# Kernel optimization log

Hardware: AMD Instinct MI355X
Metric: run time of the kernel (lower is better)

Reference implementation:

```python
import jax, jax.numpy as jnp
import numpy as np
from jax.scipy.special import erf

B, S, D = 8, 512, 512
H = 8            # num_heads per half
DH = D // 2      # 256, per-branch model dim
DFF = 2048
HOUT = 2


def _layernorm(x, g, b, eps=1e-6):
    mu = jnp.mean(x, axis=-1, keepdims=True)
    var = jnp.mean(jnp.square(x - mu), axis=-1, keepdims=True)
    return (x - mu) / jnp.sqrt(var + eps) * g + b


def _rescale_dist(w):
    one = jnp.float32(1.0)
    return (one + jnp.exp(one)) / (one + jnp.exp(one - w))


def _mha(xin, wq, bq, wk, bk, wv, bv, wo, bo, maskf, adjoin, dist):
    b, s, dm = xin.shape
    dep = dm // H
    def heads(t):
        return t.reshape(b, s, H, dep).transpose(0, 2, 1, 3)  # (b,h,s,dep)
    q = heads(xin @ wq + bq)
    k = heads(xin @ wk + bk)
    v = heads(xin @ wv + bv)
    scores = jnp.einsum('bhqd,bhkd->bhqk', q, k)
    scale = jnp.sqrt(jnp.float32(dep))
    if dist is not None:
        scores = jax.nn.relu(scores) * _rescale_dist(dist) / scale
    else:
        scores = scores / scale
    scores = scores + maskf * jnp.float32(-1e9)
    if adjoin is not None:
        scores = scores + adjoin
    attn = jax.nn.softmax(scores, axis=-1)
    out = jnp.einsum('bhqk,bhkd->bhqd', attn, v).transpose(0, 2, 1, 3).reshape(b, s, dm)
    return out @ wo + bo, attn


def setup_inputs() -> dict:
    key = jax.random.key(0)
    ks = jax.random.split(key, 32)
    init = lambda k, shp: (jax.random.normal(k, shp, dtype=jnp.float32) * 0.02)
    inp = {
        'x': jax.random.normal(ks[0], (B, S, D), dtype=jnp.float32),
        'adjoin_matrix': jax.random.normal(ks[1], (B, 1, S, S), dtype=jnp.float32),
        'dist_matrix': jax.random.uniform(ks[2], (B, 1, S, S), dtype=jnp.float32),
        # mha1 (adjoin branch)
        'wq1': init(ks[3], (DH, DH)), 'bq1': jnp.zeros((DH,), jnp.float32),
        'wk1': init(ks[4], (DH, DH)), 'bk1': jnp.zeros((DH,), jnp.float32),
        'wv1': init(ks[5], (DH, DH)), 'bv1': jnp.zeros((DH,), jnp.float32),
        'wo1': init(ks[6], (DH, DH)), 'bo1': jnp.zeros((DH,), jnp.float32),
        # mha2 (distance branch)
        'wq2': init(ks[7], (DH, DH)), 'bq2': jnp.zeros((DH,), jnp.float32),
        'wk2': init(ks[8], (DH, DH)), 'bk2': jnp.zeros((DH,), jnp.float32),
        'wv2': init(ks[9], (DH, DH)), 'bv2': jnp.zeros((DH,), jnp.float32),
        'wo2': init(ks[10], (DH, DH)), 'bo2': jnp.zeros((DH,), jnp.float32),
        # BANLayer
        'vnet_w': init(ks[11], (DH, 2 * DH)), 'vnet_b': jnp.zeros((2 * DH,), jnp.float32),
        'qnet_w': init(ks[12], (DH, 2 * DH)), 'qnet_b': jnp.zeros((2 * DH,), jnp.float32),
        'h_mat': init(ks[13], (1, HOUT, 1, 2 * DH)),
        'h_bias': init(ks[14], (1, HOUT, 1, 1)),
        'bn_gamma': jnp.ones((D,), jnp.float32), 'bn_beta': jnp.zeros((D,), jnp.float32),
        'bn_mean': jnp.zeros((D,), jnp.float32), 'bn_var': jnp.ones((D,), jnp.float32),
        # LayerNorms
        'ln1_g': jnp.ones((D,), jnp.float32), 'ln1_b': jnp.zeros((D,), jnp.float32),
        'ln2_g': jnp.ones((D,), jnp.float32), 'ln2_b': jnp.zeros((D,), jnp.float32),
        # FFN
        'ffn_w1': init(ks[15], (D, DFF)), 'ffn_b1': jnp.zeros((DFF,), jnp.float32),
        'ffn_w2': init(ks[16], (DFF, D)), 'ffn_b2': jnp.zeros((D,), jnp.float32),
        # padding mask (int -> cast), 1 = masked
        'encoder_padding_mask': jax.random.randint(ks[17], (B, 1, 1, S), 0, 2, dtype=jnp.int32),
    }
    return inp


def reference(x, adjoin_matrix, dist_matrix,
              wq1, bq1, wk1, bk1, wv1, bv1, wo1, bo1,
              wq2, bq2, wk2, bk2, wv2, bv2, wo2, bo2,
              vnet_w, vnet_b, qnet_w, qnet_b, h_mat, h_bias,
              bn_gamma, bn_beta, bn_mean, bn_var,
              ln1_g, ln1_b, ln2_g, ln2_b,
              ffn_w1, ffn_b1, ffn_w2, ffn_b2,
              encoder_padding_mask):
    maskf = encoder_padding_mask.astype(jnp.float32)
    x1, x2 = jnp.split(x, 2, axis=-1)
    # local branch: adjoin bias, no distance
    x_l, aw_local = _mha(x1, wq1, bq1, wk1, bk1, wv1, bv1, wo1, bo1, maskf, adjoin_matrix, None)
    # global branch: relu + distance rescale, no adjoin
    x_g, aw_global = _mha(x2, wq2, bq2, wk2, bk2, wv2, bv2, wo2, bo2, maskf, None, dist_matrix)
    # BANLayer (h_out=2 <= c, eval mode; p_net is identity for rows=1)
    v_ = jax.nn.relu(x_l @ vnet_w + vnet_b)   # (B,S,2*DH)
    q_ = jax.nn.relu(x_g @ qnet_w + qnet_b)
    att_maps = jnp.einsum('xhyk,bvk,bqk->bhvq', h_mat, v_, q_) + h_bias  # (B,HOUT,S,S)
    logits = jnp.einsum('bvk,bhvq,bqk->bvk', v_, att_maps, q_)           # sum over h
    logits = (logits - bn_mean) / jnp.sqrt(bn_var + 1e-3) * bn_gamma + bn_beta
    attn_output = logits * jnp.concatenate([x_l, x_g], axis=-1)
    out1 = _layernorm(x + attn_output, ln1_g, ln1_b)
    h = out1 @ ffn_w1 + ffn_b1
    h = 0.5 * h * (1.0 + erf(h / jnp.sqrt(jnp.float32(2.0))))  # exact gelu
    ffn_out = h @ ffn_w2 + ffn_b2
    out2 = _layernorm(out1 + ffn_out, ln2_g, ln2_b)
    return (out2, aw_local, aw_global)
```

## Files before the change

### kernel.cpp

```cpp
#include <hip/hip_runtime.h>
#include <hip/hip_bf16.h>

typedef __hip_bfloat16 bf16;
typedef __attribute__((ext_vector_type(8))) short bf16x8;
typedef __attribute__((ext_vector_type(4))) float f32x4;

#define BB 8
#define SS 512
#define DD 512
#define NH 8
#define DHm 256
#define DEP 32
#define DFF 2048

__device__ __forceinline__ bf16x8 cvt8(const float* p) {
  union { bf16x8 v; bf16 h[8]; } u;
  float4 f0 = *(const float4*)p, f1 = *(const float4*)(p + 4);
  u.h[0]=__float2bfloat16(f0.x); u.h[1]=__float2bfloat16(f0.y);
  u.h[2]=__float2bfloat16(f0.z); u.h[3]=__float2bfloat16(f0.w);
  u.h[4]=__float2bfloat16(f1.x); u.h[5]=__float2bfloat16(f1.y);
  u.h[6]=__float2bfloat16(f1.z); u.h[7]=__float2bfloat16(f1.w);
  return u.v;
}

template<typename TA, bool TRANSB, int ACT, typename TC>
__global__ __launch_bounds__(256)
void mfma_gemm(const TA* __restrict__ A, const float* __restrict__ B,
               const float* __restrict__ bias, TC* __restrict__ C,
               int M, int N, int K, int lda, int ldb, int ldc,
               long long sA, long long sB, long long sC)
{
  __shared__ bf16 As[64][32];
  __shared__ bf16 Bs[64][32];
  const int t = threadIdx.x;
  const int lane = t & 63, wave = t >> 6;
  const int wm = (wave & 1) << 5, wn = (wave >> 1) << 5;
  const int l15 = lane & 15, quad = lane >> 4;
  const int row0 = blockIdx.y << 6, col0 = blockIdx.x << 6;
  const TA* Ab = A + (long long)blockIdx.z * sA;
  const float* Bb = B + (long long)blockIdx.z * sB;
  TC* Cb = C + (long long)blockIdx.z * sC;

  const int ar  = t >> 2, acb = t & 3;
  const int aswz = ((acb ^ ((ar >> 1) & 3)) << 3);
  const int bn  = t & 63, bkb = t >> 6;
  const int bswz = ((bkb ^ ((bn >> 1) & 3)) << 3);

  f32x4 acc[2][2] = {};

  for (int k0 = 0; k0 < K; k0 += 32) {
    {
      union { bf16x8 v; bf16 h[8]; } u;
      if constexpr (sizeof(TA) == 2) {
        u.v = *(const bf16x8*)&Ab[(long long)(row0 + ar) * lda + k0 + (acb << 3)];
      } else {
        u.v = cvt8((const float*)&Ab[(long long)(row0 + ar) * lda + k0 + (acb << 3)]);
      }
      *(bf16x8*)&As[ar][aswz] = u.v;
    }
    if (TRANSB) {
      *(bf16x8*)&Bs[ar][aswz] = cvt8(&Bb[(long long)(col0 + ar) * ldb + k0 + (acb << 3)]);
    } else {
      union { bf16x8 v; bf16 h[8]; } u;
#pragma unroll
      for (int j = 0; j < 8; j++)
        u.h[j] = __float2bfloat16(Bb[(long long)(k0 + (bkb << 3) + j) * ldb + col0 + bn]);
      *(bf16x8*)&Bs[bn][bswz] = u.v;
    }
    __syncthreads();
    bf16x8 afr[2], bfr[2];
#pragma unroll
    for (int i = 0; i < 2; i++) {
      int m = wm + (i << 4) + l15;
      afr[i] = *(bf16x8*)&As[m][((quad ^ ((m >> 1) & 3)) << 3)];
      int n = wn + (i << 4) + l15;
      bfr[i] = *(bf16x8*)&Bs[n][((quad ^ ((n >> 1) & 3)) << 3)];
    }
#pragma unroll
    for (int i = 0; i < 2; i++)
#pragma unroll
      for (int j = 0; j < 2; j++)
        acc[i][j] = __builtin_amdgcn_mfma_f32_16x16x32_bf16(afr[i], bfr[j], acc[i][j], 0, 0, 0);
    __syncthreads();
  }

#pragma unroll
  for (int i = 0; i < 2; i++) {
#pragma unroll
    for (int j = 0; j < 2; j++) {
      int col = col0 + wn + (j << 4) + l15;
      float bv = bias ? bias[col] : 0.f;
#pragma unroll
      for (int r = 0; r < 4; r++) {
        int row = row0 + wm + (i << 4) + (quad << 2) + r;
        float v = acc[i][j][r] + bv;
        if (ACT == 1) v = fmaxf(v, 0.f);
        if (ACT == 2) v = 0.5f * v * (1.f + erff(v * 0.70710678118654752f));
        if constexpr (sizeof(TC) == 2) Cb[(long long)row * ldc + col] = __float2bfloat16(v);
        else                           Cb[(long long)row * ldc + col] = v;
      }
    }
  }
}

template<int BRANCH>
__global__ __launch_bounds__(256, 2)
void attn_mfma(const float* __restrict__ QKV, const int* __restrict__ mask,
               const float* __restrict__ extra, float* __restrict__ aw,
               float* __restrict__ ctx)
{
  const int qt = blockIdx.x, h = blockIdx.y, b = blockIdx.z;
  const int t = threadIdx.x, lane = t & 63, wave = t >> 6;
  const int l15 = lane & 15, quad = lane >> 4;
  __shared__ bf16x8 Vt[64][32];

  {
    const float* Vb = QKV + (long long)b * SS * 768 + 512 + h * 32;
    int dep = t & 31;
#pragma unroll
    for (int j8 = 0; j8 < 8; j8++) {
      int blk = (t >> 5) + (j8 << 3);
      union { bf16x8 v; bf16 hh[8]; } u;
#pragma unroll
      for (int i = 0; i < 8; i++)
        u.hh[i] = __float2bfloat16(Vb[(long long)(blk * 8 + i) * 768 + dep]);
      Vt[blk][dep] = u.v;
    }
  }

  const int q0 = qt * 64 + wave * 16;
  const float* Qb = QKV + ((long long)(b * SS + q0)) * 768 + h * 32;
  bf16x8 qfrag = cvt8(Qb + (long long)l15 * 768 + quad * 8);
  __syncthreads();

  const float scale_inv = 0.17677669529663688f;
  const float* Kb = QKV + (long long)b * SS * 768 + 256 + h * 32;
  const float* Eb = extra + ((long long)b * SS + q0) * SS;
  float sreg[32][4];
  float rmax[4] = {-1e30f, -1e30f, -1e30f, -1e30f};
#pragma unroll
  for (int kc = 0; kc < 32; kc++) {
    int kpos = kc * 16 + l15;
    bf16x8 kfrag = cvt8(Kb + (long long)kpos * 768 + quad * 8);
    f32x4 a = __builtin_amdgcn_mfma_f32_16x16x32_bf16(qfrag, kfrag, f32x4{0.f,0.f,0.f,0.f}, 0, 0, 0);
    float mval = (float)mask[b * SS + kpos] * -1e9f;
#pragma unroll
    for (int r = 0; r < 4; r++) {
      float s = a[r];
      float ev = Eb[(long long)(quad * 4 + r) * SS + kpos];
      if (BRANCH == 1) {
        s = s * scale_inv + mval + ev;
      } else {
        float resc = 3.7182818284590452f / (1.f + __expf(1.f - ev));
        s = fmaxf(s, 0.f) * resc * scale_inv + mval;
      }
      sreg[kc][r] = s;
      rmax[r] = fmaxf(rmax[r], s);
    }
  }
#pragma unroll
  for (int r = 0; r < 4; r++) {
    float v = rmax[r];
    v = fmaxf(v, __shfl_xor(v, 1, 16));
    v = fmaxf(v, __shfl_xor(v, 2, 16));
    v = fmaxf(v, __shfl_xor(v, 4, 16));
    v = fmaxf(v, __shfl_xor(v, 8, 16));
    rmax[r] = v;
  }
  float rsum[4] = {0.f, 0.f, 0.f, 0.f};
#pragma unroll
  for (int kc = 0; kc < 32; kc++)
#pragma unroll
    for (int r = 0; r < 4; r++) {
      float e = __expf(sreg[kc][r] - rmax[r]);
      sreg[kc][r] = e;
      rsum[r] += e;
    }
#pragma unroll
  for (int r = 0; r < 4; r++) {
    float v = rsum[r];
    v += __shfl_xor(v, 1, 16);
    v += __shfl_xor(v, 2, 16);
    v += __shfl_xor(v, 4, 16);
    v += __shfl_xor(v, 8, 16);
    rsum[r] = 1.f / v;
  }
  float* awp = aw + (((long long)(b * NH + h) * SS + q0)) * SS;
#pragma unroll
  for (int kc = 0; kc < 32; kc++)
#pragma unroll
    for (int r = 0; r < 4; r++)
      awp[(long long)(quad * 4 + r) * SS + kc * 16 + l15] = sreg[kc][r] * rsum[r];

  asm volatile("s_waitcnt vmcnt(0)" ::: "memory");

  f32x4 oacc[2] = {};
#pragma unroll
  for (int kc2 = 0; kc2 < 16; kc2++) {
    bf16x8 afr = cvt8(awp + (long long)l15 * SS + kc2 * 32 + quad * 8);
#pragma unroll
    for (int n = 0; n < 2; n++) {
      bf16x8 bfr = Vt[kc2 * 4 + quad][n * 16 + l15];
      oacc[n] = __builtin_amdgcn_mfma_f32_16x16x32_bf16(afr, bfr, oacc[n], 0, 0, 0);
    }
  }
#pragma unroll
  for (int n = 0; n < 2; n++)
#pragma unroll
    for (int r = 0; r < 4; r++) {
      int q = q0 + quad * 4 + r;
      ctx[(long long)(b * SS + q) * DHm + h * 32 + n * 16 + l15] = oacc[n][r];
    }
}

__global__ __launch_bounds__(256)
void pack_qkv(const float* __restrict__ wq, const float* __restrict__ wk,
              const float* __restrict__ wv, const float* __restrict__ bq,
              const float* __restrict__ bk, const float* __restrict__ bv,
              float* __restrict__ WB, float* __restrict__ BBo)
{
  int idx = blockIdx.x * 256 + threadIdx.x;
  if (idx < 768 * 256) {
    int k = idx / 768, c = idx % 768;
    int part = c >> 8, n = c & 255;
    const float* w = part == 0 ? wq : (part == 1 ? wk : wv);
    WB[idx] = w[k * 256 + n];
  } else if (idx < 768 * 256 + 768) {
    int c = idx - 768 * 256;
    int part = c >> 8, n = c & 255;
    const float* bs = part == 0 ? bq : (part == 1 ? bk : bv);
    BBo[c] = bs[n];
  }
}

__global__ __launch_bounds__(256)
void vh_kernel(const float* __restrict__ v_, const float* __restrict__ hmat,
               float* __restrict__ vh, int n)
{
  int i = blockIdx.x * 256 + threadIdx.x;
  if (i < n) {
    int c = i & (DD - 1);
    vh[i] = v_[i] * (hmat[c] + hmat[DD + c]);
  }
}

__global__ __launch_bounds__(256)
void addhb_kernel(float* __restrict__ G, const float* __restrict__ hb, int n)
{
  int i = blockIdx.x * 256 + threadIdx.x;
  if (i < n) G[i] += hb[0] + hb[1];
}

__global__ __launch_bounds__(256)
void bn_gate_ln1_kernel(const float* __restrict__ x, const float* __restrict__ vbuf,
                        const float* __restrict__ T, const float* __restrict__ xl,
                        const float* __restrict__ xg,
                        const float* __restrict__ bng, const float* __restrict__ bnb,
                        const float* __restrict__ bnm, const float* __restrict__ bnv,
                        const float* __restrict__ lng, const float* __restrict__ lnb,
                        float* __restrict__ out1)
{
  const int row = blockIdx.x;
  const int t = threadIdx.x;
  __shared__ float red[256];
  float val[2];
#pragma unroll
  for (int i = 0; i < 2; i++) {
    int c = t + i * 256;
    long long idx = (long long)row * DD + c;
    float lg = vbuf[idx] * T[idx];
    float bn = (lg - bnm[c]) / sqrtf(bnv[c] + 1e-3f) * bng[c] + bnb[c];
    float gate = (c < DHm) ? xl[(long long)row * DHm + c] : xg[(long long)row * DHm + (c - DHm)];
    val[i] = x[idx] + bn * gate;
  }
  red[t] = val[0] + val[1];
  __syncthreads();
  for (int o = 128; o > 0; o >>= 1) { if (t < o) red[t] += red[t + o]; __syncthreads(); }
  float mu = red[0] * (1.f / 512.f);
  __syncthreads();
  float d0 = val[0] - mu, d1 = val[1] - mu;
  red[t] = d0 * d0 + d1 * d1;
  __syncthreads();
  for (int o = 128; o > 0; o >>= 1) { if (t < o) red[t] += red[t + o]; __syncthreads(); }
  float inv = 1.f / sqrtf(red[0] * (1.f / 512.f) + 1e-6f);
  out1[(long long)row * DD + t]       = d0 * inv * lng[t]       + lnb[t];
  out1[(long long)row * DD + t + 256] = d1 * inv * lng[t + 256] + lnb[t + 256];
}

__global__ __launch_bounds__(256)
void ln2_kernel(const float* __restrict__ a, const float* __restrict__ b2,
                const float* __restrict__ g, const float* __restrict__ bta,
                float* __restrict__ out)
{
  const int row = blockIdx.x;
  const int t = threadIdx.x;
  __shared__ float red[256];
  float v0 = a[(long long)row * DD + t]       + b2[(long long)row * DD + t];
  float v1 = a[(long long)row * DD + t + 256] + b2[(long long)row * DD + t + 256];
  red[t] = v0 + v1;
  __syncthreads();
  for (int o = 128; o > 0; o >>= 1) { if (t < o) red[t] += red[t + o]; __syncthreads(); }
  float mu = red[0] * (1.f / 512.f);
  __syncthreads();
  float d0 = v0 - mu, d1 = v1 - mu;
  red[t] = d0 * d0 + d1 * d1;
  __syncthreads();
  for (int o = 128; o > 0; o >>= 1) { if (t < o) red[t] += red[t + o]; __syncthreads(); }
  float inv = 1.f / sqrtf(red[0] * (1.f / 512.f) + 1e-6f);
  out[(long long)row * DD + t]       = d0 * inv * g[t]       + bta[t];
  out[(long long)row * DD + t + 256] = d1 * inv * g[t + 256] + bta[t + 256];
}

extern "C" void kernel_launch(void* const* d_in, const int* in_sizes, int n_in,
                              void* d_out, int out_size, void* d_ws, size_t ws_size,
                              hipStream_t stream) {
  const float* x      = (const float*)d_in[0];
  const float* adjoin = (const float*)d_in[1];
  const float* dist   = (const float*)d_in[2];
  const float* wq1=(const float*)d_in[3],  *bq1=(const float*)d_in[4];
  const float* wk1=(const float*)d_in[5],  *bk1=(const float*)d_in[6];
  const float* wv1=(const float*)d_in[7],  *bv1=(const float*)d_in[8];
  const float* wo1=(const float*)d_in[9],  *bo1=(const float*)d_in[10];
  const float* wq2=(const float*)d_in[11], *bq2=(const float*)d_in[12];
  const float* wk2=(const float*)d_in[13], *bk2=(const float*)d_in[14];
  const float* wv2=(const float*)d_in[15], *bv2=(const float*)d_in[16];
  const float* wo2=(const float*)d_in[17], *bo2=(const float*)d_in[18];
  const float* vnet_w=(const float*)d_in[19], *vnet_b=(const float*)d_in[20];
  const float* qnet_w=(const float*)d_in[21], *qnet_b=(const float*)d_in[22];
  const float* h_mat=(const float*)d_in[23], *h_bias=(const float*)d_in[24];
  const float* bn_g=(const float*)d_in[25], *bn_b=(const float*)d_in[26];
  const float* bn_m=(const float*)d_in[27], *bn_v=(const float*)d_in[28];
  const float* ln1_g=(const float*)d_in[29], *ln1_b=(const float*)d_in[30];
  const float* ln2_g=(const float*)d_in[31], *ln2_b=(const float*)d_in[32];
  const float* ffn_w1=(const float*)d_in[33], *ffn_b1=(const float*)d_in[34];
  const float* ffn_w2=(const float*)d_in[35], *ffn_b2=(const float*)d_in[36];
  const int* mask = (const int*)d_in[37];

  float* ws = (float*)d_ws;
  const long long M1 = 1048576LL;
  float* QKV1 = ws + 0 * M1;
  float* QKV2 = ws + 3 * M1;
  float* CTX  = ws + 6 * M1;
  float* XL   = ws + 7 * M1;
  float* XG   = ws + 8 * M1;
  float* Vn   = ws + 9 * M1;
  float* Qn   = ws + 11 * M1;
  float* WB1  = ws + 13 * M1;
  float* BB1v = WB1 + 196608;
  float* WB2  = BB1v + 768;
  float* BB2v = WB2 + 196608;
  float* VH   = ws + 0 * M1;
  float* G    = ws + 3 * M1;
  float* T    = ws + 13 * M1;
  float* OUT1 = ws + 0 * M1;
  bf16*  H    = (bf16*)(ws + 3 * M1);
  float* FFNO = ws + 7 * M1;

  float* out2 = (float*)d_out;
  float* awl  = out2 + 2097152LL;
  float* awg  = awl + 16777216LL;

  const int MROWS = BB * SS;
  const long long GST = (long long)SS * SS;

  pack_qkv<<<dim3(771), 256, 0, stream>>>(wq1, wk1, wv1, bq1, bk1, bv1, WB1, BB1v);
  pack_qkv<<<dim3(771), 256, 0, stream>>>(wq2, wk2, wv2, bq2, bk2, bv2, WB2, BB2v);

  mfma_gemm<float,false,0,float><<<dim3(768/64, MROWS/64, 1), 256, 0, stream>>>(
      x, WB1, BB1v, QKV1, MROWS, 768, DHm, DD, 768, 768, 0,0,0);
  attn_mfma<1><<<dim3(8, NH, BB), 256, 0, stream>>>(QKV1, mask, adjoin, awl, CTX);
  mfma_gemm<float,false,0,float><<<dim3(DHm/64, MROWS/64, 1), 256, 0, stream>>>(
      CTX, wo1, bo1, XL, MROWS, DHm, DHm, DHm, DHm, DHm, 0,0,0);

  mfma_gemm<float,false,0,float><<<dim3(768/64, MROWS/64, 1), 256, 0, stream>>>(
      x + DHm, WB2, BB2v, QKV2, MROWS, 768, DHm, DD, 768, 768, 0,0,0);
  attn_mfma<2><<<dim3(8, NH, BB), 256, 0, stream>>>(QKV2, mask, dist, awg, CTX);
  mfma_gemm<float,false,0,float><<<dim3(DHm/64, MROWS/64, 1), 256, 0, stream>>>(
      CTX, wo2, bo2, XG, MROWS, DHm, DHm, DHm, DHm, DHm, 0,0,0);

  mfma_gemm<float,false,1,float><<<dim3(DD/64, MROWS/64, 1), 256, 0, stream>>>(
      XL, vnet_w, vnet_b, Vn, MROWS, DD, DHm, DHm, DD, DD, 0,0,0);
  mfma_gemm<float,false,1,float><<<dim3(DD/64, MROWS/64, 1), 256, 0, stream>>>(
      XG, qnet_w, qnet_b, Qn, MROWS, DD, DHm, DHm, DD, DD, 0,0,0);
  vh_kernel<<<dim3((MROWS*DD)/256), 256, 0, stream>>>(Vn, h_mat, VH, MROWS*DD);
  mfma_gemm<float,true,0,float><<<dim3(SS/64, SS/64, BB), 256, 0, stream>>>(
      VH, Qn, (const float*)nullptr, G, SS, SS, DD, DD, DD, SS, GST, GST, GST);
  addhb_kernel<<<dim3((BB*SS*SS)/256), 256, 0, stream>>>(G, h_bias, BB*SS*SS);
  mfma_gemm<float,false,0,float><<<dim3(DD/64, SS/64, BB), 256, 0, stream>>>(
      G, Qn, (const float*)nullptr, T, SS, DD, SS, SS, DD, DD, GST, GST, GST);

  bn_gate_ln1_kernel<<<dim3(MROWS), 256, 0, stream>>>(
      x, Vn, T, XL, XG, bn_g, bn_b, bn_m, bn_v, ln1_g, ln1_b, OUT1);

  mfma_gemm<float,false,2,bf16><<<dim3(DFF/64, MROWS/64, 1), 256, 0, stream>>>(
      OUT1, ffn_w1, ffn_b1, H, MROWS, DFF, DD, DD, DFF, DFF, 0,0,0);
  mfma_gemm<bf16,false,0,float><<<dim3(DD/64, MROWS/64, 1), 256, 0, stream>>>(
      H, ffn_w2, ffn_b2, FFNO, MROWS, DD, DFF, DFF, DD, DD, 0,0,0);

  ln2_kernel<<<dim3(MROWS), 256, 0, stream>>>(OUT1, FFNO, ln2_g, ln2_b, out2);
}
```

Before: 528.7 us.

## Convert pipeline to bf16 intermediates with pre-transposed weights and direct-to-LDS GEMM loads

Replaces the fp32-input GEMM with a bf16 GEMM that loads A and B tiles straight into LDS using global_load_lds. All weights and x are converted and transposed to bf16 in one pack kernel. Intermediates (QKV, ctx, Vn, Qn, G, H) are now stored as bf16, which halves memory traffic and removes per-load conversions and strided B loads. The h_bias add is folded into a GEMM epilogue, and the large GEMMs get 128x128 tiles. The cost is an extra transpose kernel for Qn and more rounding error, notably with G held in bf16.

```diff
diff --git a/kernel.cpp b/kernel.cpp
--- a/kernel.cpp
+++ b/kernel.cpp
@@ -10,8 +10,12 @@
 #define DD 512
 #define NH 8
 #define DHm 256
-#define DEP 32
 #define DFF 2048
+
+__device__ __forceinline__ void gl_lds16(const void* g, void* l) {
+  __builtin_amdgcn_global_load_lds((const __attribute__((address_space(1))) void*)g,
+                                   (__attribute__((address_space(3))) void*)l, 16, 0, 0);
+}
 
 __device__ __forceinline__ bf16x8 cvt8(const float* p) {
   union { bf16x8 v; bf16 h[8]; } u;
@@ -23,91 +27,75 @@
   return u.v;
 }
 
-template<typename TA, bool TRANSB, int ACT, typename TC>
-__global__ __launch_bounds__(256)
-void mfma_gemm(const TA* __restrict__ A, const float* __restrict__ B,
-               const float* __restrict__ bias, TC* __restrict__ C,
-               int M, int N, int K, int lda, int ldb, int ldc,
-               long long sA, long long sB, long long sC)
-{
-  __shared__ bf16 As[64][32];
-  __shared__ bf16 Bs[64][32];
-  const int t = threadIdx.x;
-  const int lane = t & 63, wave = t >> 6;
-  const int wm = (wave & 1) << 5, wn = (wave >> 1) << 5;
+template<int BM, int BN, int SMODE, int BIASM, int ACT>
+__global__ __launch_bounds__(256)
+void gemm2(const bf16* __restrict__ A, const bf16* __restrict__ B,
+           const float* __restrict__ bias, float* __restrict__ Cf,
+           bf16* __restrict__ Cb, int K, int lda, int ldb, int ldc,
+           long long sA, long long sB, long long sC)
+{
+  __shared__ bf16 As[BM * 32];
+  __shared__ bf16 Bs[BN * 32];
+  const int t = threadIdx.x, lane = t & 63, wave = t >> 6;
   const int l15 = lane & 15, quad = lane >> 4;
-  const int row0 = blockIdx.y << 6, col0 = blockIdx.x << 6;
-  const TA* Ab = A + (long long)blockIdx.z * sA;
-  const float* Bb = B + (long long)blockIdx.z * sB;
-  TC* Cb = C + (long long)blockIdx.z * sC;
-
-  const int ar  = t >> 2, acb = t & 3;
-  const int aswz = ((acb ^ ((ar >> 1) & 3)) << 3);
-  const int bn  = t & 63, bkb = t >> 6;
-  const int bswz = ((bkb ^ ((bn >> 1) & 3)) << 3);
-
-  f32x4 acc[2][2] = {};
+  constexpr int WMT = BM / 32, WNT = BN / 32;
+  const int wm = (wave & 1) * (BM / 2), wn = (wave >> 1) * (BN / 2);
+  const int row0 = blockIdx.y * BM, col0 = blockIdx.x * BN;
+  const bf16* Ab = A + (long long)blockIdx.z * sA + (long long)row0 * lda;
+  const bf16* Bb = B + (long long)blockIdx.z * sB + (long long)col0 * ldb;
+  const int srow = wave * 16 + (lane >> 2), skc = (lane & 3) << 3;
+
+  f32x4 acc[WMT][WNT] = {};
 
   for (int k0 = 0; k0 < K; k0 += 32) {
-    {
-      union { bf16x8 v; bf16 h[8]; } u;
-      if constexpr (sizeof(TA) == 2) {
-        u.v = *(const bf16x8*)&Ab[(long long)(row0 + ar) * lda + k0 + (acb << 3)];
-      } else {
-        u.v = cvt8((const float*)&Ab[(long long)(row0 + ar) * lda + k0 + (acb << 3)]);
-      }
-      *(bf16x8*)&As[ar][aswz] = u.v;
-    }
-    if (TRANSB) {
-      *(bf16x8*)&Bs[ar][aswz] = cvt8(&Bb[(long long)(col0 + ar) * ldb + k0 + (acb << 3)]);
-    } else {
-      union { bf16x8 v; bf16 h[8]; } u;
-#pragma unroll
-      for (int j = 0; j < 8; j++)
-        u.h[j] = __float2bfloat16(Bb[(long long)(k0 + (bkb << 3) + j) * ldb + col0 + bn]);
-      *(bf16x8*)&Bs[bn][bswz] = u.v;
-    }
+#pragma unroll
+    for (int j = 0; j < BM / 64; j++)
+      gl_lds16(Ab + (long long)(srow + j * 64) * lda + k0 + skc,
+               (char*)As + wave * 1024 + j * 4096);
+#pragma unroll
+    for (int j = 0; j < BN / 64; j++)
+      gl_lds16(Bb + (long long)(srow + j * 64) * ldb + k0 + skc,
+               (char*)Bs + wave * 1024 + j * 4096);
     __syncthreads();
-    bf16x8 afr[2], bfr[2];
-#pragma unroll
-    for (int i = 0; i < 2; i++) {
-      int m = wm + (i << 4) + l15;
-      afr[i] = *(bf16x8*)&As[m][((quad ^ ((m >> 1) & 3)) << 3)];
-      int n = wn + (i << 4) + l15;
-      bfr[i] = *(bf16x8*)&Bs[n][((quad ^ ((n >> 1) & 3)) << 3)];
-    }
-#pragma unroll
-    for (int i = 0; i < 2; i++)
-#pragma unroll
-      for (int j = 0; j < 2; j++)
-        acc[i][j] = __builtin_amdgcn_mfma_f32_16x16x32_bf16(afr[i], bfr[j], acc[i][j], 0, 0, 0);
+    bf16x8 af[WMT], bfr[WNT];
+#pragma unroll
+    for (int i = 0; i < WMT; i++) af[i]  = *(const bf16x8*)&As[(wm + i * 16 + l15) * 32 + quad * 8];
+#pragma unroll
+    for (int j = 0; j < WNT; j++) bfr[j] = *(const bf16x8*)&Bs[(wn + j * 16 + l15) * 32 + quad * 8];
+#pragma unroll
+    for (int i = 0; i < WMT; i++)
+#pragma unroll
+      for (int j = 0; j < WNT; j++)
+        acc[i][j] = __builtin_amdgcn_mfma_f32_16x16x32_bf16(af[i], bfr[j], acc[i][j], 0, 0, 0);
     __syncthreads();
   }
 
-#pragma unroll
-  for (int i = 0; i < 2; i++) {
-#pragma unroll
-    for (int j = 0; j < 2; j++) {
-      int col = col0 + wn + (j << 4) + l15;
-      float bv = bias ? bias[col] : 0.f;
+  float sb = 0.f;
+  if (BIASM == 2) sb = bias[0] + bias[1];
+#pragma unroll
+  for (int i = 0; i < WMT; i++)
+#pragma unroll
+    for (int j = 0; j < WNT; j++) {
+      int col = col0 + wn + j * 16 + l15;
+      float bv = (BIASM == 1) ? bias[col] : sb;
 #pragma unroll
       for (int r = 0; r < 4; r++) {
-        int row = row0 + wm + (i << 4) + (quad << 2) + r;
+        int row = row0 + wm + i * 16 + (quad << 2) + r;
         float v = acc[i][j][r] + bv;
         if (ACT == 1) v = fmaxf(v, 0.f);
         if (ACT == 2) v = 0.5f * v * (1.f + erff(v * 0.70710678118654752f));
-        if constexpr (sizeof(TC) == 2) Cb[(long long)row * ldc + col] = __float2bfloat16(v);
-        else                           Cb[(long long)row * ldc + col] = v;
+        long long ci = (long long)blockIdx.z * sC + (long long)row * ldc + col;
+        if (SMODE & 1) Cf[ci] = v;
+        if (SMODE & 2) Cb[ci] = __float2bfloat16(v);
       }
     }
-  }
 }
 
 template<int BRANCH>
 __global__ __launch_bounds__(256, 2)
-void attn_mfma(const float* __restrict__ QKV, const int* __restrict__ mask,
+void attn_mfma(const bf16* __restrict__ QKV, const int* __restrict__ mask,
                const float* __restrict__ extra, float* __restrict__ aw,
-               float* __restrict__ ctx)
+               bf16* __restrict__ ctx)
 {
   const int qt = blockIdx.x, h = blockIdx.y, b = blockIdx.z;
   const int t = threadIdx.x, lane = t & 63, wave = t >> 6;
@@ -115,7 +103,7 @@
   __shared__ bf16x8 Vt[64][32];
 
   {
-    const float* Vb = QKV + (long long)b * SS * 768 + 512 + h * 32;
+    const bf16* Vb = QKV + (long long)b * SS * 768 + 512 + h * 32;
     int dep = t & 31;
 #pragma unroll
     for (int j8 = 0; j8 < 8; j8++) {
@@ -123,25 +111,25 @@
       union { bf16x8 v; bf16 hh[8]; } u;
 #pragma unroll
       for (int i = 0; i < 8; i++)
-        u.hh[i] = __float2bfloat16(Vb[(long long)(blk * 8 + i) * 768 + dep]);
+        u.hh[i] = Vb[(long long)(blk * 8 + i) * 768 + dep];
       Vt[blk][dep] = u.v;
     }
   }
 
   const int q0 = qt * 64 + wave * 16;
-  const float* Qb = QKV + ((long long)(b * SS + q0)) * 768 + h * 32;
-  bf16x8 qfrag = cvt8(Qb + (long long)l15 * 768 + quad * 8);
+  const bf16* Qb = QKV + ((long long)(b * SS + q0)) * 768 + h * 32;
+  bf16x8 qfrag = *(const bf16x8*)(Qb + (long long)l15 * 768 + quad * 8);
   __syncthreads();
 
   const float scale_inv = 0.17677669529663688f;
-  const float* Kb = QKV + (long long)b * SS * 768 + 256 + h * 32;
+  const bf16* Kb = QKV + (long long)b * SS * 768 + 256 + h * 32;
   const float* Eb = extra + ((long long)b * SS + q0) * SS;
   float sreg[32][4];
   float rmax[4] = {-1e30f, -1e30f, -1e30f, -1e30f};
 #pragma unroll
   for (int kc = 0; kc < 32; kc++) {
     int kpos = kc * 16 + l15;
-    bf16x8 kfrag = cvt8(Kb + (long long)kpos * 768 + quad * 8);
+    bf16x8 kfrag = *(const bf16x8*)(Kb + (long long)kpos * 768 + quad * 8);
     f32x4 a = __builtin_amdgcn_mfma_f32_16x16x32_bf16(qfrag, kfrag, f32x4{0.f,0.f,0.f,0.f}, 0, 0, 0);
     float mval = (float)mask[b * SS + kpos] * -1e9f;
 #pragma unroll
@@ -209,56 +197,102 @@
 #pragma unroll
     for (int r = 0; r < 4; r++) {
       int q = q0 + quad * 4 + r;
-      ctx[(long long)(b * SS + q) * DHm + h * 32 + n * 16 + l15] = oacc[n][r];
-    }
-}
-
-__global__ __launch_bounds__(256)
-void pack_qkv(const float* __restrict__ wq, const float* __restrict__ wk,
-              const float* __restrict__ wv, const float* __restrict__ bq,
-              const float* __restrict__ bk, const float* __restrict__ bv,
-              float* __restrict__ WB, float* __restrict__ BBo)
-{
-  int idx = blockIdx.x * 256 + threadIdx.x;
-  if (idx < 768 * 256) {
-    int k = idx / 768, c = idx % 768;
-    int part = c >> 8, n = c & 255;
-    const float* w = part == 0 ? wq : (part == 1 ? wk : wv);
-    WB[idx] = w[k * 256 + n];
-  } else if (idx < 768 * 256 + 768) {
-    int c = idx - 768 * 256;
-    int part = c >> 8, n = c & 255;
-    const float* bs = part == 0 ? bq : (part == 1 ? bk : bv);
-    BBo[c] = bs[n];
-  }
-}
-
-__global__ __launch_bounds__(256)
-void vh_kernel(const float* __restrict__ v_, const float* __restrict__ hmat,
-               float* __restrict__ vh, int n)
+      ctx[(long long)(b * SS + q) * DHm + h * 32 + n * 16 + l15] = __float2bfloat16(oacc[n][r]);
+    }
+}
+
+__device__ __forceinline__ void tr_tile(const float* __restrict__ src, bf16* __restrict__ dst,
+                                        int K, int N, int tile) {
+  __shared__ float tl[32][33];
+  int tilesN = N >> 5;
+  int tk = tile / tilesN, tn = tile % tilesN;
+  int c = threadIdx.x & 31, r0 = threadIdx.x >> 5;
+#pragma unroll
+  for (int i = 0; i < 4; i++) {
+    int r = r0 + i * 8;
+    tl[r][c] = src[(long long)(tk * 32 + r) * N + tn * 32 + c];
+  }
+  __syncthreads();
+#pragma unroll
+  for (int i = 0; i < 4; i++) {
+    int r = r0 + i * 8;
+    dst[(long long)(tn * 32 + r) * K + tk * 32 + c] = __float2bfloat16(tl[c][r]);
+  }
+}
+
+__global__ __launch_bounds__(256)
+void pack_all(const float* wq1, const float* wk1, const float* wv1,
+              const float* wq2, const float* wk2, const float* wv2,
+              const float* wo1, const float* wo2,
+              const float* vnet_w, const float* qnet_w,
+              const float* ffn_w1, const float* ffn_w2,
+              const float* bq1, const float* bk1, const float* bv1,
+              const float* bq2, const float* bk2, const float* bv2,
+              const float* x,
+              bf16* WB1, bf16* WB2, bf16* woT1, bf16* woT2,
+              bf16* vnetT, bf16* qnetT, bf16* f1T, bf16* f2T,
+              float* BB1v, float* BB2v, bf16* xb)
+{
+  int blk = blockIdx.x;
+  if (blk < 64)        { tr_tile(wq1, WB1,            256, 256, blk); return; }
+  if (blk < 128)       { tr_tile(wk1, WB1 + 256*256,  256, 256, blk-64); return; }
+  if (blk < 192)       { tr_tile(wv1, WB1 + 512*256,  256, 256, blk-128); return; }
+  if (blk < 256)       { tr_tile(wq2, WB2,            256, 256, blk-192); return; }
+  if (blk < 320)       { tr_tile(wk2, WB2 + 256*256,  256, 256, blk-256); return; }
+  if (blk < 384)       { tr_tile(wv2, WB2 + 512*256,  256, 256, blk-320); return; }
+  if (blk < 448)       { tr_tile(wo1, woT1,           256, 256, blk-384); return; }
+  if (blk < 512)       { tr_tile(wo2, woT2,           256, 256, blk-448); return; }
+  if (blk < 640)       { tr_tile(vnet_w, vnetT,       256, 512, blk-512); return; }
+  if (blk < 768)       { tr_tile(qnet_w, qnetT,       256, 512, blk-640); return; }
+  if (blk < 1792)      { tr_tile(ffn_w1, f1T,         512, 2048, blk-768); return; }
+  if (blk < 2816)      { tr_tile(ffn_w2, f2T,         2048, 512, blk-1792); return; }
+  if (blk < 3840) {
+    long long i0 = (long long)(blk - 2816) * 2048 + threadIdx.x * 8;
+    *(bf16x8*)(xb + i0) = cvt8(x + i0);
+    return;
+  }
+  {
+    int b = blk - 3840;
+    const float* src = b==0?bq1 : b==1?bk1 : b==2?bv1 : b==3?bq2 : b==4?bk2 : bv2;
+    float* dst = (b < 3 ? BB1v : BB2v) + (b % 3) * 256;
+    dst[threadIdx.x] = src[threadIdx.x];
+  }
+}
+
+__global__ __launch_bounds__(256)
+void tr_qn(const bf16* __restrict__ Qn, bf16* __restrict__ QnT)
+{
+  int b = blockIdx.z, tk = blockIdx.y, tn = blockIdx.x;
+  __shared__ bf16 tl[32][33];
+  int c = threadIdx.x & 31, r0 = threadIdx.x >> 5;
+  const bf16* src = Qn + (long long)b * 512 * 512;
+  bf16* dst = QnT + (long long)b * 512 * 512;
+#pragma unroll
+  for (int i = 0; i < 4; i++) { int r = r0 + i * 8; tl[r][c] = src[(tk * 32 + r) * 512 + tn * 32 + c]; }
+  __syncthreads();
+#pragma unroll
+  for (int i = 0; i < 4; i++) { int r = r0 + i * 8; dst[(tn * 32 + r) * 512 + tk * 32 + c] = tl[c][r]; }
+}
+
+__global__ __launch_bounds__(256)
+void vh_kernel(const bf16* __restrict__ v_, const float* __restrict__ hmat,
+               bf16* __restrict__ vh, int n)
 {
   int i = blockIdx.x * 256 + threadIdx.x;
   if (i < n) {
     int c = i & (DD - 1);
-    vh[i] = v_[i] * (hmat[c] + hmat[DD + c]);
-  }
-}
-
-__global__ __launch_bounds__(256)
-void addhb_kernel(float* __restrict__ G, const float* __restrict__ hb, int n)
-{
-  int i = blockIdx.x * 256 + threadIdx.x;
-  if (i < n) G[i] += hb[0] + hb[1];
-}
-
-__global__ __launch_bounds__(256)
-void bn_gate_ln1_kernel(const float* __restrict__ x, const float* __restrict__ vbuf,
+    vh[i] = __float2bfloat16(__bfloat162float(v_[i]) * (hmat[c] + hmat[DD + c]));
+  }
+}
+
+__global__ __launch_bounds__(256)
+void bn_gate_ln1_kernel(const float* __restrict__ x, const bf16* __restrict__ vbuf,
                         const float* __restrict__ T, const float* __restrict__ xl,
                         const float* __restrict__ xg,
                         const float* __restrict__ bng, const float* __restrict__ bnb,
                         const float* __restrict__ bnm, const float* __restrict__ bnv,
                         const float* __restrict__ lng, const float* __restrict__ lnb,
-                        float* __restrict__ out1)
+                        float* __restrict__ out1, bf16* __restrict__ out1b)
 {
   const int row = blockIdx.x;
   const int t = threadIdx.x;
@@ -268,7 +302,7 @@
   for (int i = 0; i < 2; i++) {
     int c = t + i * 256;
     long long idx = (long long)row * DD + c;
-    float lg = vbuf[idx] * T[idx];
+    float lg = __bfloat162float(vbuf[idx]) * T[idx];
     float bn = (lg - bnm[c]) / sqrtf(bnv[c] + 1e-3f) * bng[c] + bnb[c];
     float gate = (c < DHm) ? xl[(long long)row * DHm + c] : xg[(long long)row * DHm + (c - DHm)];
     val[i] = x[idx] + bn * gate;
@@ -283,8 +317,12 @@
   __syncthreads();
   for (int o = 128; o > 0; o >>= 1) { if (t < o) red[t] += red[t + o]; __syncthreads(); }
   float inv = 1.f / sqrtf(red[0] * (1.f / 512.f) + 1e-6f);
-  out1[(long long)row * DD + t]       = d0 * inv * lng[t]       + lnb[t];
-  out1[(long long)row * DD + t + 256] = d1 * inv * lng[t + 256] + lnb[t + 256];
+  float o0 = d0 * inv * lng[t] + lnb[t];
+  float o1 = d1 * inv * lng[t + 256] + lnb[t + 256];
+  out1[(long long)row * DD + t] = o0;
+  out1[(long long)row * DD + t + 256] = o1;
+  out1b[(long long)row * DD + t] = __float2bfloat16(o0);
+  out1b[(long long)row * DD + t + 256] = __float2bfloat16(o1);
 }
 
 __global__ __launch_bounds__(256)
@@ -336,66 +374,80 @@
   const float* ffn_w2=(const float*)d_in[35], *ffn_b2=(const float*)d_in[36];
   const int* mask = (const int*)d_in[37];
 
-  float* ws = (float*)d_ws;
-  const long long M1 = 1048576LL;
-  float* QKV1 = ws + 0 * M1;
-  float* QKV2 = ws + 3 * M1;
-  float* CTX  = ws + 6 * M1;
-  float* XL   = ws + 7 * M1;
-  float* XG   = ws + 8 * M1;
-  float* Vn   = ws + 9 * M1;
-  float* Qn   = ws + 11 * M1;
-  float* WB1  = ws + 13 * M1;
-  float* BB1v = WB1 + 196608;
-  float* WB2  = BB1v + 768;
-  float* BB2v = WB2 + 196608;
-  float* VH   = ws + 0 * M1;
-  float* G    = ws + 3 * M1;
-  float* T    = ws + 13 * M1;
-  float* OUT1 = ws + 0 * M1;
-  bf16*  H    = (bf16*)(ws + 3 * M1);
-  float* FFNO = ws + 7 * M1;
+  char* base = (char*)d_ws;
+  size_t off = 0;
+  auto alloc = [&](size_t bytes) { char* p = base + off; off += (bytes + 255) & ~(size_t)255; return p; };
+  bf16*  xb    = (bf16*) alloc(4096LL*512*2);
+  bf16*  WB1   = (bf16*) alloc(768*256*2);
+  bf16*  WB2   = (bf16*) alloc(768*256*2);
+  float* BB1v  = (float*)alloc(768*4);
+  float* BB2v  = (float*)alloc(768*4);
+  bf16*  woT1  = (bf16*) alloc(256*256*2);
+  bf16*  woT2  = (bf16*) alloc(256*256*2);
+  bf16*  vnetT = (bf16*) alloc(512*256*2);
+  bf16*  qnetT = (bf16*) alloc(512*256*2);
+  bf16*  f1T   = (bf16*) alloc(2048*512*2);
+  bf16*  f2T   = (bf16*) alloc(512*2048*2);
+  bf16*  QKV1  = (bf16*) alloc(4096LL*768*2);
+  bf16*  QKV2  = (bf16*) alloc(4096LL*768*2);
+  bf16*  CTX   = (bf16*) alloc(4096LL*256*2);
+  float* XL    = (float*)alloc(4096LL*256*4);
+  float* XG    = (float*)alloc(4096LL*256*4);
+  bf16*  XLb   = (bf16*) alloc(4096LL*256*2);
+  bf16*  XGb   = (bf16*) alloc(4096LL*256*2);
+  bf16*  Vn    = (bf16*) alloc(4096LL*512*2);
+  bf16*  Qn    = (bf16*) alloc(4096LL*512*2);
+  bf16*  QnT   = (bf16*) alloc(4096LL*512*2);
+  bf16*  VH    = (bf16*) alloc(4096LL*512*2);
+  bf16*  G     = (bf16*) alloc(8LL*512*512*2);
+  float* T     = (float*)alloc(4096LL*512*4);
+  float* OUT1  = (float*)alloc(4096LL*512*4);
+  bf16*  OUT1b = (bf16*) alloc(4096LL*512*2);
+  bf16*  H     = (bf16*) alloc(4096LL*2048*2);
+  float* FFNO  = (float*)alloc(4096LL*512*4);
 
   float* out2 = (float*)d_out;
   float* awl  = out2 + 2097152LL;
   float* awg  = awl + 16777216LL;
 
-  const int MROWS = BB * SS;
+  const int MR = BB * SS;
   const long long GST = (long long)SS * SS;
 
-  pack_qkv<<<dim3(771), 256, 0, stream>>>(wq1, wk1, wv1, bq1, bk1, bv1, WB1, BB1v);
-  pack_qkv<<<dim3(771), 256, 0, stream>>>(wq2, wk2, wv2, bq2, bk2, bv2, WB2, BB2v);
-
-  mfma_gemm<float,false,0,float><<<dim3(768/64, MROWS/64, 1), 256, 0, stream>>>(
-      x, WB1, BB1v, QKV1, MROWS, 768, DHm, DD, 768, 768, 0,0,0);
+  pack_all<<<dim3(3846), 256, 0, stream>>>(
+      wq1, wk1, wv1, wq2, wk2, wv2, wo1, wo2, vnet_w, qnet_w, ffn_w1, ffn_w2,
+      bq1, bk1, bv1, bq2, bk2, bv2, x,
+      WB1, WB2, woT1, woT2, vnetT, qnetT, f1T, f2T, BB1v, BB2v, xb);
+
+  gemm2<128,128,2,1,0><<<dim3(6, 32, 1), 256, 0, stream>>>(
+      xb,       WB1, BB1v, nullptr, QKV1, 256, 512, 256, 768, 0, 0, 0);
+  gemm2<128,128,2,1,0><<<dim3(6, 32, 1), 256, 0, stream>>>(
+      xb + 256, WB2, BB2v, nullptr, QKV2, 256, 512, 256, 768, 0, 0, 0);
+
   attn_mfma<1><<<dim3(8, NH, BB), 256, 0, stream>>>(QKV1, mask, adjoin, awl, CTX);
-  mfma_gemm<float,false,0,float><<<dim3(DHm/64, MROWS/64, 1), 256, 0, stream>>>(
-      CTX, wo1, bo1, XL, MROWS, DHm, DHm, DHm, DHm, DHm, 0,0,0);
-
-  mfma_gemm<float,false,0,float><<<dim3(768/64, MROWS/64, 1), 256, 0, stream>>>(
-      x + DHm, WB2, BB2v, QKV2, MROWS, 768, DHm, DD, 768, 768, 0,0,0);
+  gemm2<64,64,3,1,0><<<dim3(4, 64, 1), 256, 0, stream>>>(
+      CTX, woT1, bo1, XL, XLb, 256, 256, 256, 256, 0, 0, 0);
   attn_mfma<2><<<dim3(8, NH, BB), 256, 0, stream>>>(QKV2, mask, dist, awg, CTX);
-  mfma_gemm<float,false,0,float><<<dim3(DHm/64, MROWS/64, 1), 256, 0, stream>>>(
-      CTX, wo2, bo2, XG, MROWS, DHm, DHm, DHm, DHm, DHm, 0,0,0);
-
-  mfma_gemm<float,false,1,float><<<dim3(DD/64, MROWS/64, 1), 256, 0, stream>>>(
-      XL, vnet_w, vnet_b, Vn, MROWS, DD, DHm, DHm, DD, DD, 0,0,0);
-  mfma_gemm<float,false,1,float><<<dim3(DD/64, MROWS/64, 1), 256, 0, stream>>>(
-      XG, qnet_w, qnet_b, Qn, MROWS, DD, DHm, DHm, DD, DD, 0,0,0);
-  vh_kernel<<<dim3((MROWS*DD)/256), 256, 0, stream>>>(Vn, h_mat, VH, MROWS*DD);
-  mfma_gemm<float,true,0,float><<<dim3(SS/64, SS/64, BB), 256, 0, stream>>>(
-      VH, Qn, (const float*)nullptr, G, SS, SS, DD, DD, DD, SS, GST, GST, GST);
-  addhb_kernel<<<dim3((BB*SS*SS)/256), 256, 0, stream>>>(G, h_bias, BB*SS*SS);
-  mfma_gemm<float,false,0,float><<<dim3(DD/64, SS/64, BB), 256, 0, stream>>>(
-      G, Qn, (const float*)nullptr, T, SS, DD, SS, SS, DD, DD, GST, GST, GST);
-
-  bn_gate_ln1_kernel<<<dim3(MROWS), 256, 0, stream>>>(
-      x, Vn, T, XL, XG, bn_g, bn_b, bn_m, bn_v, ln1_g, ln1_b, OUT1);
-
-  mfma_gemm<float,false,2,bf16><<<dim3(DFF/64, MROWS/64, 1), 256, 0, stream>>>(
-      OUT1, ffn_w1, ffn_b1, H, MROWS, DFF, DD, DD, DFF, DFF, 0,0,0);
-  mfma_gemm<bf16,false,0,float><<<dim3(DD/64, MROWS/64, 1), 256, 0, stream>>>(
-      H, ffn_w2, ffn_b2, FFNO, MROWS, DD, DFF, DFF, DD, DD, 0,0,0);
-
-  ln2_kernel<<<dim3(MROWS), 256, 0, stream>>>(OUT1, FFNO, ln2_g, ln2_b, out2);
-}
+  gemm2<64,64,3,1,0><<<dim3(4, 64, 1), 256, 0, stream>>>(
+      CTX, woT2, bo2, XG, XGb, 256, 256, 256, 256, 0, 0, 0);
+
+  gemm2<64,64,2,1,1><<<dim3(8, 64, 1), 256, 0, stream>>>(
+      XLb, vnetT, vnet_b, nullptr, Vn, 256, 256, 256, 512, 0, 0, 0);
+  gemm2<64,64,2,1,1><<<dim3(8, 64, 1), 256, 0, stream>>>(
+      XGb, qnetT, qnet_b, nullptr, Qn, 256, 256, 256, 512, 0, 0, 0);
+  vh_kernel<<<dim3((MR * DD) / 256), 256, 0, stream>>>(Vn, h_mat, VH, MR * DD);
+  tr_qn<<<dim3(16, 16, BB), 256, 0, stream>>>(Qn, QnT);
+  gemm2<64,64,2,2,0><<<dim3(8, 8, BB), 256, 0, stream>>>(
+      VH, Qn, h_bias, nullptr, G, 512, 512, 512, 512, GST, GST, GST);
+  gemm2<64,64,1,0,0><<<dim3(8, 8, BB), 256, 0, stream>>>(
+      G, QnT, nullptr, T, nullptr, 512, 512, 512, 512, GST, GST, GST);
+
+  bn_gate_ln1_kernel<<<dim3(MR), 256, 0, stream>>>(
+      x, Vn, T, XL, XG, bn_g, bn_b, bn_m, bn_v, ln1_g, ln1_b, OUT1, OUT1b);
+
+  gemm2<128,128,2,1,2><<<dim3(16, 32, 1), 256, 0, stream>>>(
+      OUT1b, f1T, ffn_b1, nullptr, H, 512, 512, 512, 2048, 0, 0, 0);
+  gemm2<64,64,1,1,0><<<dim3(8, 64, 1), 256, 0, stream>>>(
+      H, f2T, ffn_b2, FFNO, nullptr, 2048, 2048, 2048, 512, 0, 0, 0);
+
+  ln2_kernel<<<dim3(MR), 256, 0, stream>>>(OUT1, FFNO, ln2_g, ln2_b, out2);
+}
```

After: 451.1 us. -14.7%, faster.
